# Kernel tuning notes

Measured on AMD Instinct MI355X. Metric: run time of the kernel, lower is better.

## Reference

```python
import jax, jax.numpy as jnp
import numpy as np

D_MODEL = 1024
N_HEADS = 16
HEAD_DIM = D_MODEL // N_HEADS
SCALE = HEAD_DIM ** (-0.5)
D_GRAPH = 8
B, N = 4, 1024
NEG_INF = -1.0e9


def setup_inputs() -> dict:
    key = jax.random.key(0)
    ks = jax.random.split(key, 8)
    std = (2.0 / (5.0 * D_MODEL)) ** 0.5
    q = jax.random.normal(ks[0], (B, N, D_MODEL), dtype=jnp.float32)
    k = jax.random.normal(ks[1], (B, N, D_MODEL), dtype=jnp.float32)
    v = jax.random.normal(ks[2], (B, N, D_MODEL), dtype=jnp.float32)
    mask = jax.random.randint(ks[3], (B, N), 0, 2).astype(bool)
    graphormer_dists = jax.random.uniform(ks[4], (B, N, N, D_GRAPH), dtype=jnp.float32)
    weights = std * jax.random.normal(ks[5], (4 * D_MODEL, D_MODEL), dtype=jnp.float32)
    biases = jnp.zeros((4 * D_MODEL,), dtype=jnp.float32)
    w_graph = std * jax.random.normal(ks[6], (N_HEADS, D_GRAPH), dtype=jnp.float32)
    return {"q": q, "k": k, "v": v, "mask": mask,
            "graphormer_dists": graphormer_dists,
            "weights": weights, "biases": biases, "w_graph": w_graph}


def _proj(x, weights, biases, start, end):
    # F.linear with a slice of the fused [4*d_model, d_model] weight
    return x @ weights[start:end].T + biases[start:end]


def _split_heads(x):
    b, n, _ = x.shape
    return x.reshape(b, n, N_HEADS, HEAD_DIM).transpose(0, 2, 1, 3)  # bhnd


def reference(q, k, v, mask, graphormer_dists, weights, biases, w_graph):
    b, n, _ = q.shape
    qh = _split_heads(_proj(q, weights, biases, 0, D_MODEL))
    kh = _split_heads(_proj(k, weights, biases, D_MODEL, 2 * D_MODEL))
    vh = _split_heads(_proj(v, weights, biases, 2 * D_MODEL, 3 * D_MODEL))
    # dot-product scores, scaled
    att = jnp.einsum('bhnd,bhmd->bhnm', qh, kh) * SCALE
    # graphormer bias: Linear(d_graph -> n_heads), then permute to bhnm
    att = att + jnp.einsum('bnmp,hp->bhnm', graphormer_dists, w_graph)
    # mask fills along the QUERY dim (mask[:,None,:,None]), as in the source
    att = jnp.where(mask[:, None, :, None], NEG_INF, att)
    att = jax.nn.softmax(att, axis=-1)
    # dropout p=0.0 (eval): identity
    out = jnp.einsum('bhnm,bhmd->bhnd', att, vh)
    out = out.transpose(0, 2, 1, 3).reshape(b, n, D_MODEL)
    out = _proj(out, weights, biases, 3 * D_MODEL, 4 * D_MODEL)
    return out, att
```

## Files before the change

### kernel.cpp

```cpp
#include <hip/hip_runtime.h>
#include <hip/hip_bf16.h>

#define SEQ      1024
#define BATCH    4
#define NHEADS   16
#define HDIM     64
#define DMODEL   1024
#define DGRAPH   8
#define QK_SCALE 0.125f
#define PCONST   0.0009765625f

typedef __attribute__((ext_vector_type(8))) short bf16x8;
typedef __attribute__((ext_vector_type(4))) short bf16x4;
typedef __attribute__((ext_vector_type(4))) float f32x4;

__device__ __forceinline__ void split_bf16(float x, short& hi, short& lo) {
    unsigned u = __float_as_uint(x);
    hi = (short)(u >> 16);
    float hf = __uint_as_float(u & 0xffff0000u);
    lo = (short)(__float_as_uint(x - hf) >> 16);
}

__device__ __forceinline__ short f2bf_rne(float x) {
    unsigned u = __float_as_uint(x);
    u += 0x7fffu + ((u >> 16) & 1u);
    return (short)(u >> 16);
}

__global__ __launch_bounds__(256) void prep_split(
    const float* __restrict__ X, short* __restrict__ Hi, short* __restrict__ Lo)
{
    const int idx = blockIdx.x * 256 + threadIdx.x;
    const float* p = X + (size_t)idx * 8;
    float4 u0 = *(const float4*)p;
    float4 u1 = *(const float4*)(p + 4);
    float v[8] = {u0.x, u0.y, u0.z, u0.w, u1.x, u1.y, u1.z, u1.w};
    bf16x8 hv, lv;
#pragma unroll
    for (int j = 0; j < 8; ++j) {
        short h, s; split_bf16(v[j], h, s);
        hv[j] = h; lv[j] = s;
    }
    *(bf16x8*)(Hi + (size_t)idx * 8) = hv;
    *(bf16x8*)(Lo + (size_t)idx * 8) = lv;
}

template<int INMODE, int OUTMODE>
__global__ __launch_bounds__(256) void proj_mfma(
    const float* __restrict__ X,
    const short* __restrict__ Xhi, const short* __restrict__ Xlo,
    const short* __restrict__ Whi, const short* __restrict__ Wlo,
    const float* __restrict__ bias,
    float* __restrict__ Yf,
    short* __restrict__ Yhi,
    short* __restrict__ Ylo,
    float scale)
{
    constexpr int LDK = 40;
    __shared__ short Ah[128 * LDK];
    __shared__ short Al[128 * LDK];
    __shared__ short Bh[64 * LDK];
    __shared__ short Bl[64 * LDK];

    const int t   = threadIdx.x;
    const int w   = t >> 6;
    const int l   = t & 63;
    const int l15 = l & 15;
    const int lk  = (l >> 4) * 8;
    const int m0  = blockIdx.y * 128;
    const int c0  = blockIdx.x * 64;
    const int wr  = (w >> 1) * 64;
    const int wc  = (w & 1) * 32;

    const int srow = t >> 2;
    const int skg  = t & 3;

    f32x4 acc[4][2];
#pragma unroll
    for (int i = 0; i < 4; ++i)
#pragma unroll
        for (int j = 0; j < 2; ++j) acc[i][j] = f32x4{0.f, 0.f, 0.f, 0.f};

    float  xa[2][8];
    bf16x8 xh[2], xl[2];
    bf16x8 wh, wl;

    if constexpr (INMODE == 0) {
#pragma unroll
        for (int i = 0; i < 2; ++i) {
            const float* p = X + (size_t)(m0 + srow + i * 64) * DMODEL + skg * 8;
            float4 u0 = *(const float4*)p;
            float4 u1 = *(const float4*)(p + 4);
            xa[i][0] = u0.x; xa[i][1] = u0.y; xa[i][2] = u0.z; xa[i][3] = u0.w;
            xa[i][4] = u1.x; xa[i][5] = u1.y; xa[i][6] = u1.z; xa[i][7] = u1.w;
        }
    } else {
#pragma unroll
        for (int i = 0; i < 2; ++i) {
            const size_t off = (size_t)(m0 + srow + i * 64) * DMODEL + skg * 8;
            xh[i] = *(const bf16x8*)(Xhi + off);
            xl[i] = *(const bf16x8*)(Xlo + off);
        }
    }
    {
        const size_t off = (size_t)(c0 + srow) * DMODEL + skg * 8;
        wh = *(const bf16x8*)(Whi + off);
        wl = *(const bf16x8*)(Wlo + off);
    }

    for (int kt = 0; kt < 32; ++kt) {
        if constexpr (INMODE == 0) {
#pragma unroll
            for (int i = 0; i < 2; ++i) {
                bf16x8 hv, lv;
#pragma unroll
                for (int j = 0; j < 8; ++j) {
                    short h, s; split_bf16(xa[i][j], h, s);
                    hv[j] = h; lv[j] = s;
                }
                *(bf16x8*)(Ah + (srow + i * 64) * LDK + skg * 8) = hv;
                *(bf16x8*)(Al + (srow + i * 64) * LDK + skg * 8) = lv;
            }
        } else {
#pragma unroll
            for (int i = 0; i < 2; ++i) {
                *(bf16x8*)(Ah + (srow + i * 64) * LDK + skg * 8) = xh[i];
                *(bf16x8*)(Al + (srow + i * 64) * LDK + skg * 8) = xl[i];
            }
        }
        *(bf16x8*)(Bh + srow * LDK + skg * 8) = wh;
        *(bf16x8*)(Bl + srow * LDK + skg * 8) = wl;
        __syncthreads();

        if (kt + 1 < 32) {
            const int k0 = (kt + 1) * 32;
            if constexpr (INMODE == 0) {
#pragma unroll
                for (int i = 0; i < 2; ++i) {
                    const float* p = X + (size_t)(m0 + srow + i * 64) * DMODEL + k0 + skg * 8;
                    float4 u0 = *(const float4*)p;
                    float4 u1 = *(const float4*)(p + 4);
                    xa[i][0] = u0.x; xa[i][1] = u0.y; xa[i][2] = u0.z; xa[i][3] = u0.w;
                    xa[i][4] = u1.x; xa[i][5] = u1.y; xa[i][6] = u1.z; xa[i][7] = u1.w;
                }
            } else {
#pragma unroll
                for (int i = 0; i < 2; ++i) {
                    const size_t off = (size_t)(m0 + srow + i * 64) * DMODEL + k0 + skg * 8;
                    xh[i] = *(const bf16x8*)(Xhi + off);
                    xl[i] = *(const bf16x8*)(Xlo + off);
                }
            }
            const size_t off = (size_t)(c0 + srow) * DMODEL + k0 + skg * 8;
            wh = *(const bf16x8*)(Whi + off);
            wl = *(const bf16x8*)(Wlo + off);
        }

        bf16x8 ah[4], alo[4], bh[2], blo[2];
#pragma unroll
        for (int fm = 0; fm < 4; ++fm) {
            const int off = (wr + fm * 16 + l15) * LDK + lk;
            ah[fm]  = *(const bf16x8*)(Ah + off);
            alo[fm] = *(const bf16x8*)(Al + off);
        }
#pragma unroll
        for (int fn = 0; fn < 2; ++fn) {
            const int off = (wc + fn * 16 + l15) * LDK + lk;
            bh[fn]  = *(const bf16x8*)(Bh + off);
            blo[fn] = *(const bf16x8*)(Bl + off);
        }
#pragma unroll
        for (int fm = 0; fm < 4; ++fm)
#pragma unroll
            for (int fn = 0; fn < 2; ++fn) {
                acc[fm][fn] = __builtin_amdgcn_mfma_f32_16x16x32_bf16(
                    ah[fm], bh[fn], acc[fm][fn], 0, 0, 0);
                acc[fm][fn] = __builtin_amdgcn_mfma_f32_16x16x32_bf16(
                    ah[fm], blo[fn], acc[fm][fn], 0, 0, 0);
                acc[fm][fn] = __builtin_amdgcn_mfma_f32_16x16x32_bf16(
                    alo[fm], bh[fn], acc[fm][fn], 0, 0, 0);
            }
        __syncthreads();
    }

#pragma unroll
    for (int fm = 0; fm < 4; ++fm)
#pragma unroll
        for (int fn = 0; fn < 2; ++fn) {
            const int c = c0 + wc + fn * 16 + l15;
            const float bb = bias[c];
#pragma unroll
            for (int r = 0; r < 4; ++r) {
                const int m = m0 + wr + fm * 16 + (l >> 4) * 4 + r;
                const float v = (acc[fm][fn][r] + bb) * scale;
                if constexpr (OUTMODE == 0) {
                    Yf[(size_t)m * DMODEL + c] = v;
                } else {
                    const int b_ = m >> 10, n = m & 1023;
                    const int h = c >> 6, d = c & 63;
                    short hi, lo; split_bf16(v, hi, lo);
                    if constexpr (OUTMODE == 2) {
                        const size_t idx =
                            ((size_t)((b_ * NHEADS + h) * SEQ + n)) * HDIM + d;
                        Yhi[idx] = hi; Ylo[idx] = lo;
                    } else {
                        const size_t idx =
                            ((size_t)((b_ * NHEADS + h) * HDIM + d)) * SEQ + n;
                        Yhi[idx] = hi; Ylo[idx] = lo;
                    }
                }
            }
        }
}

__global__ __launch_bounds__(256) void graph_bias_kernel(
    const float* __restrict__ dists,
    const float* __restrict__ wg,
    const int* __restrict__ mask,
    float* __restrict__ attL,
    float* __restrict__ rowSum)
{
    const int n = blockIdx.x & 1023;
    const int b = blockIdx.x >> 10;
    const int t = threadIdx.x;
    if (t < NHEADS)
        rowSum[(size_t)(b * NHEADS + t) * SEQ + n] = 0.f;
    if (mask[b * SEQ + n]) return;

    __shared__ float wgs[NHEADS * DGRAPH];
    if (t < NHEADS * DGRAPH) wgs[t] = wg[t];
    __syncthreads();

    const int m = t * 4;
    const float* dp = dists + (((size_t)(b * SEQ + n)) * SEQ + m) * DGRAPH;
    float d[4][8];
#pragma unroll
    for (int i = 0; i < 8; ++i) {
        float4 v = *reinterpret_cast<const float4*>(dp + i * 4);
        d[i >> 1][(i & 1) * 4 + 0] = v.x; d[i >> 1][(i & 1) * 4 + 1] = v.y;
        d[i >> 1][(i & 1) * 4 + 2] = v.z; d[i >> 1][(i & 1) * 4 + 3] = v.w;
    }
#pragma unroll
    for (int h = 0; h < NHEADS; ++h) {
        float ov[4];
#pragma unroll
        for (int jm = 0; jm < 4; ++jm) {
            float s = 0.f;
#pragma unroll
            for (int p = 0; p < DGRAPH; ++p)
                s = fmaf(d[jm][p], wgs[h * DGRAPH + p], s);
            ov[jm] = s;
        }
        float4 o; o.x = ov[0]; o.y = ov[1]; o.z = ov[2]; o.w = ov[3];
        *reinterpret_cast<float4*>(
            attL + (((size_t)((b * NHEADS + h) * SEQ + n)) * SEQ + m)) = o;
    }
}

__global__ __launch_bounds__(256) void qk_mfma(
    const short* __restrict__ Qhi, const short* __restrict__ Qlo,
    const short* __restrict__ Khi, const short* __restrict__ Klo,
    const int* __restrict__ mask,
    float* __restrict__ attL,
    float* __restrict__ rowSum)
{
    constexpr int LDK = 72;
    __shared__ short sQh[128 * LDK];
    __shared__ short sQl[128 * LDK];
    __shared__ short sKh[128 * LDK];
    __shared__ short sKl[128 * LDK];
    __shared__ int maskS[128];

    const int bid = blockIdx.x;
    const int bh  = ((bid >> 9) << 3) | (bid & 7);
    const int j   = (bid >> 3) & 63;
    const int m0  = (j & 7) * 128;
    const int n0  = (j >> 3) * 128;
    const int b   = bh >> 4;

    const int t   = threadIdx.x;
    const int w   = t >> 6;
    const int l   = t & 63;
    const int l15 = l & 15;
    const int lk  = (l >> 4) * 8;

    if (t < 128) maskS[t] = mask[b * SEQ + n0 + t];

#pragma unroll
    for (int it = 0; it < 4; ++it) {
        const int f   = t + it * 256;
        const int row = f >> 3;
        const int c8  = f & 7;
        const size_t gq = ((size_t)bh * SEQ + n0 + row) * HDIM + c8 * 8;
        const size_t gk = ((size_t)bh * SEQ + m0 + row) * HDIM + c8 * 8;
        const int lo = row * LDK + c8 * 8;
        *(bf16x8*)(sQh + lo) = *(const bf16x8*)(Qhi + gq);
        *(bf16x8*)(sQl + lo) = *(const bf16x8*)(Qlo + gq);
        *(bf16x8*)(sKh + lo) = *(const bf16x8*)(Khi + gk);
        *(bf16x8*)(sKl + lo) = *(const bf16x8*)(Klo + gk);
    }
    __syncthreads();

    const int nr  = (w >> 1) * 64;
    const int mcw = (w & 1) * 64;

    f32x4 acc[4][4];
    {
        const float* bb = attL + ((size_t)bh * SEQ + n0 + nr + (l >> 4) * 4) * SEQ
                          + m0 + mcw + l15;
#pragma unroll
        for (int fm = 0; fm < 4; ++fm)
#pragma unroll
            for (int r = 0; r < 4; ++r) {
                const int nloc = nr + fm * 16 + (l >> 4) * 4 + r;
                const bool mk = maskS[nloc] != 0;
#pragma unroll
                for (int fn = 0; fn < 4; ++fn)
                    acc[fm][fn][r] =
                        mk ? 0.f : bb[(size_t)(fm * 16 + r) * SEQ + fn * 16];
            }
    }

#pragma unroll
    for (int ks = 0; ks < 2; ++ks) {
        bf16x8 ah[4], alo[4], bhv[4], blo[4];
#pragma unroll
        for (int fm = 0; fm < 4; ++fm) {
            const int off = (nr + fm * 16 + l15) * LDK + ks * 32 + lk;
            ah[fm]  = *(const bf16x8*)(sQh + off);
            alo[fm] = *(const bf16x8*)(sQl + off);
        }
#pragma unroll
        for (int fn = 0; fn < 4; ++fn) {
            const int off = (mcw + fn * 16 + l15) * LDK + ks * 32 + lk;
            bhv[fn] = *(const bf16x8*)(sKh + off);
            blo[fn] = *(const bf16x8*)(sKl + off);
        }
#pragma unroll
        for (int fm = 0; fm < 4; ++fm)
#pragma unroll
            for (int fn = 0; fn < 4; ++fn) {
                acc[fm][fn] = __builtin_amdgcn_mfma_f32_16x16x32_bf16(
                    ah[fm], bhv[fn], acc[fm][fn], 0, 0, 0);
                acc[fm][fn] = __builtin_amdgcn_mfma_f32_16x16x32_bf16(
                    ah[fm], blo[fn], acc[fm][fn], 0, 0, 0);
                acc[fm][fn] = __builtin_amdgcn_mfma_f32_16x16x32_bf16(
                    alo[fm], bhv[fn], acc[fm][fn], 0, 0, 0);
            }
    }

#pragma unroll
    for (int fm = 0; fm < 4; ++fm)
#pragma unroll
        for (int r = 0; r < 4; ++r) {
            const int nloc = nr + fm * 16 + (l >> 4) * 4 + r;
            const bool msk = maskS[nloc] != 0;
            float* rowp = attL + ((size_t)bh * SEQ + n0 + nloc) * SEQ + m0 + mcw + l15;
            float s = 0.f;
#pragma unroll
            for (int fn = 0; fn < 4; ++fn) {
                const float e = __expf(acc[fm][fn][r]);
                s += e;
                if (!msk) rowp[fn * 16] = e;
            }
            s += __shfl_xor(s, 1); s += __shfl_xor(s, 2);
            s += __shfl_xor(s, 4); s += __shfl_xor(s, 8);
            if (!msk && l15 == 0)
                atomicAdd(rowSum + (size_t)bh * SEQ + n0 + nloc, s);
        }
}

__global__ __launch_bounds__(256) void pv_mfma(
    float* __restrict__ attL,
    const short* __restrict__ VThi,
    const short* __restrict__ VTlo,
    const int* __restrict__ mask,
    const float* __restrict__ rowSum,
    short* __restrict__ AOhi,
    short* __restrict__ AOlo)
{
    constexpr int LDP = 72;
    __shared__ short pHi[128 * LDP];
    __shared__ short sVh[64 * LDP];
    __shared__ short sVl[64 * LDP];
    __shared__ float rowInv[128];
    __shared__ int   maskS[128];

    const int bid  = blockIdx.x;
    const int flat = (bid & 63) * 8 + (bid >> 6);
    const int n0   = (flat & 7) * 128;
    const int h    = (flat >> 3) & 15;
    const int b    = flat >> 7;

    const int t   = threadIdx.x;
    const int w   = t >> 6;
    const int l   = t & 63;
    const int l15 = l & 15;
    const int lk  = (l >> 4) * 8;
    const int bh  = b * NHEADS + h;
    float* Lbase = attL + ((size_t)bh * SEQ + n0) * SEQ;

    if (t < 128) {
        const int mk = mask[b * SEQ + n0 + t];
        maskS[t] = mk;
        rowInv[t] = mk ? 0.f : 1.0f / rowSum[(size_t)bh * SEQ + n0 + t];
    }
    __syncthreads();

    const int nr = (w >> 1) * 64;
    const int dc = (w & 1) * 32;

    f32x4 acc[4][2];
#pragma unroll
    for (int i = 0; i < 4; ++i)
#pragma unroll
        for (int j = 0; j < 2; ++j) acc[i][j] = f32x4{0.f, 0.f, 0.f, 0.f};

    float4 sreg[8];
#pragma unroll
    for (int i = 0; i < 8; ++i) sreg[i] = make_float4(0.f, 0.f, 0.f, 0.f);
#pragma unroll
    for (int i = 0; i < 8; ++i) {
        const int f4 = t + i * 256;
        const int row = f4 >> 4, mq = f4 & 15;
        if (!maskS[row])
            sreg[i] = *reinterpret_cast<const float4*>(
                Lbase + (size_t)row * SEQ + mq * 4);
    }

    for (int mc = 0; mc < 16; ++mc) {
#pragma unroll
        for (int i = 0; i < 8; ++i) {
            const int f4 = t + i * 256;
            const int row = f4 >> 4, mq = f4 & 15;
            float4 p4;
            if (maskS[row]) {
                p4.x = PCONST; p4.y = PCONST; p4.z = PCONST; p4.w = PCONST;
            } else {
                const float iv = rowInv[row];
                p4.x = sreg[i].x * iv; p4.y = sreg[i].y * iv;
                p4.z = sreg[i].z * iv; p4.w = sreg[i].w * iv;
            }
            *reinterpret_cast<float4*>(
                Lbase + (size_t)row * SEQ + mc * 64 + mq * 4) = p4;
            bf16x4 hv;
            hv[0] = f2bf_rne(p4.x); hv[1] = f2bf_rne(p4.y);
            hv[2] = f2bf_rne(p4.z); hv[3] = f2bf_rne(p4.w);
            *(bf16x4*)(pHi + row * LDP + mq * 4) = hv;
        }
#pragma unroll
        for (int i = 0; i < 2; ++i) {
            const int f = t + i * 256;
            const int d = f >> 3, m8 = f & 7;
            const size_t src = ((size_t)bh * HDIM + d) * SEQ + mc * 64 + m8 * 8;
            *(bf16x8*)(sVh + d * LDP + m8 * 8) = *(const bf16x8*)(VThi + src);
            *(bf16x8*)(sVl + d * LDP + m8 * 8) = *(const bf16x8*)(VTlo + src);
        }
        __syncthreads();

        if (mc + 1 < 16) {
#pragma unroll
            for (int i = 0; i < 8; ++i) {
                const int f4 = t + i * 256;
                const int row = f4 >> 4, mq = f4 & 15;
                if (!maskS[row])
                    sreg[i] = *reinterpret_cast<const float4*>(
                        Lbase + (size_t)row * SEQ + (mc + 1) * 64 + mq * 4);
            }
        }

#pragma unroll
        for (int ks = 0; ks < 2; ++ks) {
            bf16x8 ah[4], bhv[2], blo[2];
#pragma unroll
            for (int fm = 0; fm < 4; ++fm) {
                const int off = (nr + fm * 16 + l15) * LDP + ks * 32 + lk;
                ah[fm] = *(const bf16x8*)(pHi + off);
            }
#pragma unroll
            for (int fn = 0; fn < 2; ++fn) {
                const int off = (dc + fn * 16 + l15) * LDP + ks * 32 + lk;
                bhv[fn] = *(const bf16x8*)(sVh + off);
                blo[fn] = *(const bf16x8*)(sVl + off);
            }
#pragma unroll
            for (int fm = 0; fm < 4; ++fm)
#pragma unroll
                for (int fn = 0; fn < 2; ++fn) {
                    acc[fm][fn] = __builtin_amdgcn_mfma_f32_16x16x32_bf16(
                        ah[fm], bhv[fn], acc[fm][fn], 0, 0, 0);
                    acc[fm][fn] = __builtin_amdgcn_mfma_f32_16x16x32_bf16(
                        ah[fm], blo[fn], acc[fm][fn], 0, 0, 0);
                }
        }
        __syncthreads();
    }

#pragma unroll
    for (int fm = 0; fm < 4; ++fm)
#pragma unroll
        for (int fn = 0; fn < 2; ++fn) {
            const int dd = dc + fn * 16 + l15;
#pragma unroll
            for (int r = 0; r < 4; ++r) {
                const int n = n0 + nr + fm * 16 + (l >> 4) * 4 + r;
                const size_t idx =
                    ((size_t)(b * SEQ + n)) * DMODEL + h * HDIM + dd;
                short hi, lo; split_bf16(acc[fm][fn][r], hi, lo);
                AOhi[idx] = hi; AOlo[idx] = lo;
            }
        }
}

extern "C" void kernel_launch(void* const* d_in, const int* in_sizes, int n_in,
                              void* d_out, int out_size, void* d_ws, size_t ws_size,
                              hipStream_t stream) {
    const float* q       = (const float*)d_in[0];
    const float* k       = (const float*)d_in[1];
    const float* v       = (const float*)d_in[2];
    const int*   mask    = (const int*)d_in[3];
    const float* dists   = (const float*)d_in[4];
    const float* weights = (const float*)d_in[5];
    const float* biases  = (const float*)d_in[6];
    const float* wg      = (const float*)d_in[7];

    float* out  = (float*)d_out;
    float* attL = out + (size_t)BATCH * SEQ * DMODEL;

    const size_t HSZ = (size_t)BATCH * NHEADS * SEQ * HDIM;
    const size_t WSZ = (size_t)4 * DMODEL * DMODEL;
    short* Qhi  = (short*)d_ws;
    short* Qlo  = Qhi + HSZ;
    short* Khi  = Qlo + HSZ;
    short* Klo  = Khi + HSZ;
    short* VThi = Klo + HSZ;
    short* VTlo = VThi + HSZ;
    short* Whi  = VTlo + HSZ;
    short* Wlo  = Whi + WSZ;
    short* AOhi = Qhi;
    short* AOlo = Qlo;
    float* rowSum = out;

    const size_t DD = (size_t)DMODEL * DMODEL;

    prep_split<<<(int)(WSZ / 8 / 256), 256, 0, stream>>>(weights, Whi, Wlo);

    graph_bias_kernel<<<BATCH * SEQ, 256, 0, stream>>>(dists, wg, mask, attL, rowSum);

    dim3 gProj(DMODEL / 64, (BATCH * SEQ) / 128);
    proj_mfma<0, 2><<<gProj, 256, 0, stream>>>(q, nullptr, nullptr,
        Whi, Wlo, biases, nullptr, Qhi, Qlo, QK_SCALE);
    proj_mfma<0, 2><<<gProj, 256, 0, stream>>>(k, nullptr, nullptr,
        Whi + DD, Wlo + DD, biases + DMODEL, nullptr, Khi, Klo, 1.0f);
    proj_mfma<0, 3><<<gProj, 256, 0, stream>>>(v, nullptr, nullptr,
        Whi + 2 * DD, Wlo + 2 * DD, biases + 2 * DMODEL, nullptr, VThi, VTlo, 1.0f);

    qk_mfma<<<(SEQ / 128) * (SEQ / 128) * BATCH * NHEADS, 256, 0, stream>>>(
        Qhi, Qlo, Khi, Klo, mask, attL, rowSum);

    pv_mfma<<<(SEQ / 128) * NHEADS * BATCH, 256, 0, stream>>>(
        attL, VThi, VTlo, mask, rowSum, AOhi, AOlo);

    proj_mfma<1, 0><<<gProj, 256, 0, stream>>>(nullptr, AOhi, AOlo,
        Whi + 3 * DD, Wlo + 3 * DD, biases + 3 * DMODEL, out, nullptr, nullptr, 1.0f);
}
```

Measured before the change: 418.7 us.

## Fuse graphormer bias computation into QK kernel and remap block order

Removes the separate graph-bias kernel, which wrote a full fp32 bias tensor into the attention buffer only for the QK kernel to read it back. The QK kernel now reads the graph distances directly and does the 8-wide dot product with that head's weights when it initializes its accumulators. Blocks are remapped so heads sharing the same (b, n, m) tile are scheduled near each other, hoping the distance tile gets reused from cache. In exchange, distances may be re-read once per head, and the per-lane strided 32-byte loads are less coalesced; a small kernel now zeroes the row sums.

Result: slower. 533.6 us (+27.4%).

```diff
diff --git a/kernel.cpp b/kernel.cpp
--- a/kernel.cpp
+++ b/kernel.cpp
@@ -25,6 +25,11 @@
     unsigned u = __float_as_uint(x);
     u += 0x7fffu + ((u >> 16) & 1u);
     return (short)(u >> 16);
+}
+
+__global__ void zero_f32(float* p, int n) {
+    int i = blockIdx.x * 256 + threadIdx.x;
+    if (i < n) p[i] = 0.f;
 }
 
 __global__ __launch_bounds__(256) void prep_split(
@@ -213,53 +218,11 @@
         }
 }
 
-__global__ __launch_bounds__(256) void graph_bias_kernel(
-    const float* __restrict__ dists,
-    const float* __restrict__ wg,
-    const int* __restrict__ mask,
-    float* __restrict__ attL,
-    float* __restrict__ rowSum)
-{
-    const int n = blockIdx.x & 1023;
-    const int b = blockIdx.x >> 10;
-    const int t = threadIdx.x;
-    if (t < NHEADS)
-        rowSum[(size_t)(b * NHEADS + t) * SEQ + n] = 0.f;
-    if (mask[b * SEQ + n]) return;
-
-    __shared__ float wgs[NHEADS * DGRAPH];
-    if (t < NHEADS * DGRAPH) wgs[t] = wg[t];
-    __syncthreads();
-
-    const int m = t * 4;
-    const float* dp = dists + (((size_t)(b * SEQ + n)) * SEQ + m) * DGRAPH;
-    float d[4][8];
-#pragma unroll
-    for (int i = 0; i < 8; ++i) {
-        float4 v = *reinterpret_cast<const float4*>(dp + i * 4);
-        d[i >> 1][(i & 1) * 4 + 0] = v.x; d[i >> 1][(i & 1) * 4 + 1] = v.y;
-        d[i >> 1][(i & 1) * 4 + 2] = v.z; d[i >> 1][(i & 1) * 4 + 3] = v.w;
-    }
-#pragma unroll
-    for (int h = 0; h < NHEADS; ++h) {
-        float ov[4];
-#pragma unroll
-        for (int jm = 0; jm < 4; ++jm) {
-            float s = 0.f;
-#pragma unroll
-            for (int p = 0; p < DGRAPH; ++p)
-                s = fmaf(d[jm][p], wgs[h * DGRAPH + p], s);
-            ov[jm] = s;
-        }
-        float4 o; o.x = ov[0]; o.y = ov[1]; o.z = ov[2]; o.w = ov[3];
-        *reinterpret_cast<float4*>(
-            attL + (((size_t)((b * NHEADS + h) * SEQ + n)) * SEQ + m)) = o;
-    }
-}
-
 __global__ __launch_bounds__(256) void qk_mfma(
     const short* __restrict__ Qhi, const short* __restrict__ Qlo,
     const short* __restrict__ Khi, const short* __restrict__ Klo,
+    const float* __restrict__ dists,
+    const float* __restrict__ wg,
     const int* __restrict__ mask,
     float* __restrict__ attL,
     float* __restrict__ rowSum)
@@ -271,12 +234,14 @@
     __shared__ short sKl[128 * LDK];
     __shared__ int maskS[128];
 
-    const int bid = blockIdx.x;
-    const int bh  = ((bid >> 9) << 3) | (bid & 7);
-    const int j   = (bid >> 3) & 63;
-    const int m0  = (j & 7) * 128;
-    const int n0  = (j >> 3) * 128;
-    const int b   = bh >> 4;
+    const int bid  = blockIdx.x;
+    const int flat = (bid & 511) * 8 + (bid >> 9);
+    const int h    = flat & 15;
+    const int j    = (flat >> 4) & 63;
+    const int b    = flat >> 10;
+    const int m0   = (j & 7) * 128;
+    const int n0   = (j >> 3) * 128;
+    const int bh   = b * NHEADS + h;
 
     const int t   = threadIdx.x;
     const int w   = t >> 6;
@@ -304,22 +269,39 @@
     const int nr  = (w >> 1) * 64;
     const int mcw = (w & 1) * 64;
 
+    float wgv[8];
+    {
+        float4 w0 = *(const float4*)(wg + h * DGRAPH);
+        float4 w1 = *(const float4*)(wg + h * DGRAPH + 4);
+        wgv[0] = w0.x; wgv[1] = w0.y; wgv[2] = w0.z; wgv[3] = w0.w;
+        wgv[4] = w1.x; wgv[5] = w1.y; wgv[6] = w1.z; wgv[7] = w1.w;
+    }
+
     f32x4 acc[4][4];
-    {
-        const float* bb = attL + ((size_t)bh * SEQ + n0 + nr + (l >> 4) * 4) * SEQ
-                          + m0 + mcw + l15;
-#pragma unroll
-        for (int fm = 0; fm < 4; ++fm)
-#pragma unroll
-            for (int r = 0; r < 4; ++r) {
-                const int nloc = nr + fm * 16 + (l >> 4) * 4 + r;
-                const bool mk = maskS[nloc] != 0;
-#pragma unroll
-                for (int fn = 0; fn < 4; ++fn)
-                    acc[fm][fn][r] =
-                        mk ? 0.f : bb[(size_t)(fm * 16 + r) * SEQ + fn * 16];
-            }
-    }
+#pragma unroll
+    for (int fm = 0; fm < 4; ++fm)
+#pragma unroll
+        for (int r = 0; r < 4; ++r) {
+            const int nloc = nr + fm * 16 + (l >> 4) * 4 + r;
+            if (maskS[nloc]) {
+#pragma unroll
+                for (int fn = 0; fn < 4; ++fn) acc[fm][fn][r] = 0.f;
+                continue;
+            }
+            const float* dp = dists +
+                (((size_t)(b * SEQ + n0 + nloc)) * SEQ + m0 + mcw + l15) * DGRAPH;
+#pragma unroll
+            for (int fn = 0; fn < 4; ++fn) {
+                float4 d0 = *(const float4*)(dp + fn * 16 * DGRAPH);
+                float4 d1 = *(const float4*)(dp + fn * 16 * DGRAPH + 4);
+                float s = 0.f;
+                s = fmaf(d0.x, wgv[0], s); s = fmaf(d0.y, wgv[1], s);
+                s = fmaf(d0.z, wgv[2], s); s = fmaf(d0.w, wgv[3], s);
+                s = fmaf(d1.x, wgv[4], s); s = fmaf(d1.y, wgv[5], s);
+                s = fmaf(d1.z, wgv[6], s); s = fmaf(d1.w, wgv[7], s);
+                acc[fm][fn][r] = s;
+            }
+        }
 
 #pragma unroll
     for (int ks = 0; ks < 2; ++ks) {
@@ -542,10 +524,10 @@
     float* rowSum = out;
 
     const size_t DD = (size_t)DMODEL * DMODEL;
+    const int NROWS = BATCH * NHEADS * SEQ;
 
     prep_split<<<(int)(WSZ / 8 / 256), 256, 0, stream>>>(weights, Whi, Wlo);
-
-    graph_bias_kernel<<<BATCH * SEQ, 256, 0, stream>>>(dists, wg, mask, attL, rowSum);
+    zero_f32<<<(NROWS + 255) / 256, 256, 0, stream>>>(rowSum, NROWS);
 
     dim3 gProj(DMODEL / 64, (BATCH * SEQ) / 128);
     proj_mfma<0, 2><<<gProj, 256, 0, stream>>>(q, nullptr, nullptr,
@@ -556,7 +538,7 @@
         Whi + 2 * DD, Wlo + 2 * DD, biases + 2 * DMODEL, nullptr, VThi, VTlo, 1.0f);
 
     qk_mfma<<<(SEQ / 128) * (SEQ / 128) * BATCH * NHEADS, 256, 0, stream>>>(
-        Qhi, Qlo, Khi, Klo, mask, attL, rowSum);
+        Qhi, Qlo, Khi, Klo, dists, wg, mask, attL, rowSum);
 
     pv_mfma<<<(SEQ / 128) * NHEADS * BATCH, 256, 0, stream>>>(
         attL, VThi, VTlo, mask, rowSum, AOhi, AOlo);
```
